# Kernel tuning notes

Hardware: AMD Instinct MI355X
Metric: run time of the kernel (lower is better)

Reference implementation:

```python
import jax, jax.numpy as jnp
import numpy as np

EMBED = 128      # embed_dim
D2 = 128         # state_dim_2d
ENC = 128        # encoder_state_dim
L_IN = 64        # max_input_len
L_OUT = 64       # max_output_len
VOCAB = 32000
BATCH = 32
CELL_IN = 2 * ENC + EMBED  # 384


def setup_inputs() -> dict:
    key = jax.random.key(0)
    ks = jax.random.split(key, 17)
    w = lambda k, shape: jax.random.normal(k, shape, jnp.float32) * 0.05
    return {
        "x": jax.random.randint(ks[0], (L_IN, BATCH), 0, VOCAB),
        "embedding": w(ks[1], (VOCAB, EMBED)),
        # bidirectional encoder LSTM, torch gate order (i, f, g, o)
        "enc_Wih_f": w(ks[2], (4 * ENC, EMBED)),
        "enc_Whh_f": w(ks[3], (4 * ENC, ENC)),
        "enc_bih_f": w(ks[4], (4 * ENC,)),
        "enc_bhh_f": w(ks[5], (4 * ENC,)),
        "enc_Wih_b": w(ks[6], (4 * ENC, EMBED)),
        "enc_Whh_b": w(ks[7], (4 * ENC, ENC)),
        "enc_bih_b": w(ks[8], (4 * ENC,)),
        "enc_bhh_b": w(ks[9], (4 * ENC,)),
        # 2D-LSTM cell: gates (i, f, o, lambda, g)
        "Wx": w(ks[10], (5 * D2, CELL_IN)),
        "bx": w(ks[11], (5 * D2,)),
        "Ws": w(ks[12], (5 * D2, 2 * D2)),
        "bs": w(ks[13], (5 * D2,)),
        "logW": w(ks[14], (VOCAB, D2)),
        "logb": w(ks[15], (VOCAB,)),
    }


def _forward(x, embedding, enc_Wih_f, enc_Whh_f, enc_bih_f, enc_bhh_f,
             enc_Wih_b, enc_Whh_b, enc_bih_b, enc_bhh_b,
             Wx, bx, Ws, bs, logW, logb):
    emb = embedding[x]  # [L_in, B, E]
    Lin, B = emb.shape[0], emb.shape[1]

    def lstm_dir(Wih, Whh, bih, bhh, reverse):
        H = Whh.shape[1]
        def step(carry, e):
            h, c = carry
            z = e @ Wih.T + bih + h @ Whh.T + bhh
            i, f, g, o = jnp.split(z, 4, axis=-1)
            c = jax.nn.sigmoid(f) * c + jax.nn.sigmoid(i) * jnp.tanh(g)
            h = jax.nn.sigmoid(o) * jnp.tanh(c)
            return (h, c), h
        init = (jnp.zeros((B, H), emb.dtype), jnp.zeros((B, H), emb.dtype))
        _, hs = jax.lax.scan(step, init, emb, reverse=reverse)
        return hs

    # bidirectional encoder hidden states: [L_in, B, 2*ENC]
    h = jnp.concatenate([
        lstm_dir(enc_Wih_f, enc_Whh_f, enc_bih_f, enc_bhh_f, False),
        lstm_dir(enc_Wih_b, enc_Whh_b, enc_bih_b, enc_bhh_b, True),
    ], axis=-1)

    D = Ws.shape[1] // 2

    def cell(y_i, h_j, s_hor, s_ver, c_hor, c_ver):
        xj = jnp.concatenate([y_i, h_j], axis=-1)
        z = xj @ Wx.T + bx + jnp.concatenate([s_hor, s_ver], axis=-1) @ Ws.T + bs
        i, f, o, l, g = jnp.split(z, 5, axis=-1)
        i, f, o, l = (jax.nn.sigmoid(t) for t in (i, f, o, l))
        g = jnp.tanh(g)
        c = f * (l * c_hor + (1.0 - l) * c_ver) + i * g
        s = o * jnp.tanh(c)
        return c, s

    z0 = jnp.zeros((B, D), h.dtype)
    zrow = jnp.zeros((Lin, B, D), h.dtype)
    y0 = jnp.zeros((B, embedding.shape[1]), h.dtype)

    def outer(carry, _):
        y_i, s_row, c_row = carry
        def inner(hc, inp):
            s_hor, c_hor = hc
            h_j, s_ver, c_ver = inp
            c, s = cell(y_i, h_j, s_hor, s_ver, c_hor, c_ver)
            return (s, c), (s, c)
        (s_last, _), (s_new, c_new) = jax.lax.scan(inner, (z0, z0), (h, s_row, c_row))
        probs = jax.nn.softmax(s_last @ logW.T + logb, axis=-1)
        y_next = embedding[jnp.argmax(probs, axis=-1)]
        return (y_next, s_new, c_new), probs

    _, y_hat = jax.lax.scan(outer, (y0, zrow, zrow), None, length=L_OUT)
    return y_hat  # [L_out, B, V]


def reference(x, embedding, enc_Wih_f, enc_Whh_f, enc_bih_f, enc_bhh_f,
              enc_Wih_b, enc_Whh_b, enc_bih_b, enc_bhh_b,
              Wx, bx, Ws, bs, logW, logb):
    return _forward(x, embedding, enc_Wih_f, enc_Whh_f, enc_bih_f, enc_bhh_f,
                    enc_Wih_b, enc_Whh_b, enc_bih_b, enc_bhh_b,
                    Wx, bx, Ws, bs, logW, logb)
```

## Files before the change

kernel.cpp:

```cpp
#include <hip/hip_runtime.h>
#include <cstdint>
#include <cstddef>

#define LI 64
#define LO 64
#define NB 32
#define E  128
#define ENC 128
#define D2 128
#define VOC 32000
#define CIN 384
#define G5 640
#define G4 512
#define NCK 256
#define VPC 125

__device__ __forceinline__ float sigf(float x) { return 1.0f / (1.0f + __expf(-x)); }
__device__ __forceinline__ float tanhf_(float x) {
  float e = __expf(2.0f * x);
  return 1.0f - 2.0f / (e + 1.0f);
}

__global__ __launch_bounds__(512) void k_embed_encpre(
    const int* __restrict__ x, const float* __restrict__ embed,
    const float* __restrict__ Wf, const float* __restrict__ bihf, const float* __restrict__ bhhf,
    const float* __restrict__ Wb, const float* __restrict__ bihb, const float* __restrict__ bhhb,
    float* __restrict__ Xf, float* __restrict__ Xb)
{
  int t = blockIdx.x >> 2, bg = (blockIdx.x & 3) * 8;
  __shared__ float4 embs[8][E/4];
  int tid = threadIdx.x;
  for (int idx = tid; idx < 8 * E; idx += 512) {
    int bb = idx >> 7, e = idx & 127;
    int tok = x[t * NB + bg + bb];
    ((float*)embs[bb])[e] = embed[(size_t)tok * E + e];
  }
  __syncthreads();
  int gd = tid;
  for (int dir = 0; dir < 2; ++dir) {
    const float4* wrow = (const float4*)((dir ? Wb : Wf) + (size_t)gd * E);
    float bias = dir ? (bihb[gd] + bhhb[gd]) : (bihf[gd] + bhhf[gd]);
    float acc[8];
    #pragma unroll
    for (int r = 0; r < 8; ++r) acc[r] = bias;
    for (int q = 0; q < E/4; ++q) {
      float4 w = wrow[q];
      #pragma unroll
      for (int r = 0; r < 8; ++r) {
        float4 e4 = embs[r][q];
        acc[r] += w.x*e4.x + w.y*e4.y + w.z*e4.z + w.w*e4.w;
      }
    }
    float* X = dir ? Xb : Xf;
    #pragma unroll
    for (int r = 0; r < 8; ++r)
      X[(size_t)(t * NB + bg + r) * G4 + gd] = acc[r];
  }
}

__global__ __launch_bounds__(512) void k_encoder(
    const float* __restrict__ Xf, const float* __restrict__ Xb,
    const float* __restrict__ Whhf, const float* __restrict__ Whhb,
    float* __restrict__ henc)
{
  int b = blockIdx.x >> 1, dir = blockIdx.x & 1;
  const float* X   = dir ? Xb   : Xf;
  const float* Whh = dir ? Whhb : Whhf;
  int tid = threadIdx.x;
  float4 w[ENC/4];
  {
    const float4* wrow = (const float4*)(Whh + (size_t)tid * ENC);
    #pragma unroll
    for (int q = 0; q < ENC/4; ++q) w[q] = wrow[q];
  }
  __shared__ float4 hb4[ENC/4];
  __shared__ float zb[G4];
  if (tid < ENC/4) hb4[tid] = make_float4(0.f, 0.f, 0.f, 0.f);
  float c = 0.0f;
  __syncthreads();
  for (int st = 0; st < LI; ++st) {
    int t = dir ? (LI - 1 - st) : st;
    float acc = X[(size_t)(t * NB + b) * G4 + tid];
    #pragma unroll
    for (int q = 0; q < ENC/4; ++q) {
      float4 h4 = hb4[q];
      float4 ww = w[q];
      acc += ww.x*h4.x + ww.y*h4.y + ww.z*h4.z + ww.w*h4.w;
    }
    zb[tid] = acc;
    __syncthreads();
    if (tid < ENC) {
      float zi = zb[tid], zf = zb[ENC + tid], zg = zb[2*ENC + tid], zo = zb[3*ENC + tid];
      c = sigf(zf) * c + sigf(zi) * tanhf_(zg);
      float h = sigf(zo) * tanhf_(c);
      ((float*)hb4)[tid] = h;
      henc[(size_t)(t * NB + b) * (2*ENC) + dir*ENC + tid] = h;
    }
    __syncthreads();
  }
}

__global__ __launch_bounds__(640) void k_hx(
    const float* __restrict__ henc, const float* __restrict__ Wx,
    const float* __restrict__ bx, const float* __restrict__ bs,
    float* __restrict__ Hx, float* __restrict__ Vpre0)
{
  int rowbase = blockIdx.x * 8;
  __shared__ float4 hh[8][(2*ENC)/4];
  int tid = threadIdx.x;
  for (int idx = tid; idx < 8 * 2 * ENC; idx += 640) {
    int rr = idx >> 8, k = idx & 255;
    ((float*)hh[rr])[k] = henc[(size_t)(rowbase + rr) * (2*ENC) + k];
  }
  __syncthreads();
  int gd = tid;
  const float4* wrow = (const float4*)(Wx + (size_t)gd * CIN + E);
  float bias = bx[gd] + bs[gd];
  float acc[8];
  #pragma unroll
  for (int r = 0; r < 8; ++r) acc[r] = bias;
  for (int q = 0; q < (2*ENC)/4; ++q) {
    float4 w = wrow[q];
    #pragma unroll
    for (int r = 0; r < 8; ++r) {
      float4 h4 = hh[r][q];
      acc[r] += w.x*h4.x + w.y*h4.y + w.z*h4.z + w.w*h4.w;
    }
  }
  #pragma unroll
  for (int r = 0; r < 8; ++r) {
    size_t o = (size_t)(rowbase + r) * G5 + gd;
    Hx[o] = acc[r];
    Vpre0[o] = acc[r];
  }
}

__global__ __launch_bounds__(640) void k_row(
    int row,
    const float* __restrict__ embed, const float* __restrict__ Wx,
    const float* __restrict__ Ws,
    const float* __restrict__ Vpre,
    const float* __restrict__ cprev,
    float* __restrict__ scur, float* __restrict__ ccur,
    const float* __restrict__ ckval, const int* __restrict__ ckidx)
{
  int b = blockIdx.x, tid = threadIdx.x;
  __shared__ float zb[G5];
  __shared__ float4 sb4[D2/4];
  __shared__ float ybuf[E];
  __shared__ int tokls;
  float yxr = 0.0f;
  if (row > 0) {
    if (tid < 64) {
      float bv = -3.4e38f; int bi = 0x7fffffff;
      #pragma unroll
      for (int cc = 0; cc < 4; ++cc) {
        int c = tid + 64 * cc;
        float v = ckval[b * NCK + c];
        int   id = ckidx[b * NCK + c];
        if (v > bv || (v == bv && id < bi)) { bv = v; bi = id; }
      }
      #pragma unroll
      for (int off = 1; off < 64; off <<= 1) {
        float ov = __shfl_xor(bv, off);
        int   oi = __shfl_xor(bi, off);
        if (ov > bv || (ov == bv && oi < bi)) { bv = ov; bi = oi; }
      }
      if (tid == 0) tokls = bi;
    }
    __syncthreads();
    int tok = tokls;
    if (tid < E) ybuf[tid] = embed[(size_t)tok * E + tid];
    __syncthreads();
    const float4* wy = (const float4*)(Wx + (size_t)tid * CIN);
    const float4* y4 = (const float4*)ybuf;
    float a = 0.0f;
    #pragma unroll
    for (int q = 0; q < E/4; ++q) {
      float4 w = wy[q], y = y4[q];
      a += w.x*y.x + w.y*y.y + w.z*y.z + w.w*y.w;
    }
    yxr = a;
  }
  float4 w[D2/4];
  {
    const float4* wrow = (const float4*)(Ws + (size_t)tid * (2*D2));
    #pragma unroll
    for (int q = 0; q < D2/4; ++q) w[q] = wrow[q];
  }
  if (tid < D2/4) sb4[tid] = make_float4(0.f, 0.f, 0.f, 0.f);
  float chor = 0.0f;
  __syncthreads();
  float vnext = Vpre[(size_t)(0 * NB + b) * G5 + tid];
  float cvn = (tid < D2) ? cprev[(size_t)(0 * NB + b) * D2 + tid] : 0.0f;
  for (int j = 0; j < LI; ++j) {
    float acc = yxr + vnext;
    if (j < LI - 1) vnext = Vpre[(size_t)((j + 1) * NB + b) * G5 + tid];
    #pragma unroll
    for (int q = 0; q < D2/4; ++q) {
      float4 s4 = sb4[q];
      float4 ww = w[q];
      acc += ww.x*s4.x + ww.y*s4.y + ww.z*s4.z + ww.w*s4.w;
    }
    zb[tid] = acc;
    __syncthreads();
    if (tid < D2) {
      float zi = zb[tid], zf = zb[D2 + tid], zo = zb[2*D2 + tid],
            zl = zb[3*D2 + tid], zg = zb[4*D2 + tid];
      float cv = cvn;
      if (j < LI - 1) cvn = cprev[(size_t)((j + 1) * NB + b) * D2 + tid];
      float ii = sigf(zi), ff = sigf(zf), oo = sigf(zo), ll = sigf(zl);
      float gg = tanhf_(zg);
      float c = ff * (ll * chor + (1.0f - ll) * cv) + ii * gg;
      float s = oo * tanhf_(c);
      chor = c;
      ((float*)sb4)[tid] = s;
      size_t o = (size_t)(j * NB + b) * D2 + tid;
      ccur[o] = c;
      scur[o] = s;
    }
    __syncthreads();
  }
}

__global__ __launch_bounds__(256) void k_fused(
    int row,
    const float* __restrict__ scur,
    const float* __restrict__ logW, const float* __restrict__ logb,
    const float* __restrict__ Ws, const float* __restrict__ Hx,
    float* __restrict__ Vnxt,
    float* __restrict__ lgcur, float* __restrict__ ckvalcur, int* __restrict__ ckidxcur,
    const float* __restrict__ lgprev, const float* __restrict__ ckvalprev,
    float* __restrict__ dout)
{
  int bid = blockIdx.x, tid = threadIdx.x;
  if (bid < 256) {
    if (row >= 64) return;
    int b = tid >> 3, r = tid & 7;
    const float4* sp = (const float4*)(scur + (size_t)(63 * NB + b) * D2 + r * 16);
    float4 s0 = sp[0], s1 = sp[1], s2 = sp[2], s3 = sp[3];
    float bm = -3.4e38f; int bmi = 0;
    int v0 = bid * VPC;
    for (int k = 0; k < VPC; ++k) {
      int v = v0 + k;
      const float4* lw = (const float4*)(logW + (size_t)v * D2 + r * 16);
      float4 a0 = lw[0], a1 = lw[1], a2 = lw[2], a3 = lw[3];
      float sum = a0.x*s0.x + a0.y*s0.y + a0.z*s0.z + a0.w*s0.w
                + a1.x*s1.x + a1.y*s1.y + a1.z*s1.z + a1.w*s1.w
                + a2.x*s2.x + a2.y*s2.y + a2.z*s2.z + a2.w*s2.w
                + a3.x*s3.x + a3.y*s3.y + a3.z*s3.z + a3.w*s3.w;
      sum += __shfl_xor(sum, 1);
      sum += __shfl_xor(sum, 2);
      sum += __shfl_xor(sum, 4);
      if (r == 0) {
        float lg = sum + logb[v];
        lgcur[(size_t)b * VOC + v] = lg;
        if (lg > bm) { bm = lg; bmi = v; }
      }
    }
    if (r == 0) {
      ckvalcur[b * NCK + bid] = bm;
      ckidxcur[b * NCK + bid] = bmi;
    }
  } else if (bid < 512) {
    if (row >= 63) return;
    int rowbase = (bid - 256) * 8;
    __shared__ float4 sr[8][D2/4];
    for (int idx = tid; idx < 8 * D2; idx += 256) {
      int rr = idx >> 7, k = idx & 127;
      ((float*)sr[rr])[k] = scur[(size_t)(rowbase + rr) * D2 + k];
    }
    __syncthreads();
    for (int gd = tid; gd < G5; gd += 256) {
      const float4* wrow = (const float4*)(Ws + (size_t)gd * (2*D2) + D2);
      float acc[8];
      #pragma unroll
      for (int rr = 0; rr < 8; ++rr) acc[rr] = 0.0f;
      for (int q = 0; q < D2/4; ++q) {
        float4 ww = wrow[q];
        #pragma unroll
        for (int rr = 0; rr < 8; ++rr) {
          float4 s4 = sr[rr][q];
          acc[rr] += ww.x*s4.x + ww.y*s4.y + ww.z*s4.z + ww.w*s4.w;
        }
      }
      #pragma unroll
      for (int rr = 0; rr < 8; ++rr) {
        size_t o = (size_t)(rowbase + rr) * G5 + gd;
        Vnxt[o] = Hx[o] + acc[rr];
      }
    }
  } else {
    if (row == 0) return;
    int b = bid - 512;
    __shared__ float red[256];
    red[tid] = ckvalprev[b * NCK + tid];
    __syncthreads();
    for (int off = 128; off > 0; off >>= 1) {
      if (tid < off) red[tid] = fmaxf(red[tid], red[tid + off]);
      __syncthreads();
    }
    float M = red[0];
    __syncthreads();
    const float* lg = lgprev + (size_t)b * VOC;
    float S = 0.0f;
    for (int k = 0; k < VPC; ++k) S += __expf(lg[tid + 256 * k] - M);
    red[tid] = S;
    __syncthreads();
    for (int off = 128; off > 0; off >>= 1) {
      if (tid < off) red[tid] += red[tid + off];
      __syncthreads();
    }
    float rinv = 1.0f / red[0];
    float* o = dout + ((size_t)(row - 1) * NB + b) * VOC;
    for (int k = 0; k < VPC; ++k) {
      int v = tid + 256 * k;
      o[v] = __expf(lg[v] - M) * rinv;
    }
  }
}

extern "C" void kernel_launch(void* const* d_in, const int* in_sizes, int n_in,
                              void* d_out, int out_size, void* d_ws, size_t ws_size,
                              hipStream_t stream)
{
  (void)in_sizes; (void)n_in; (void)out_size; (void)ws_size;
  const int*   x     = (const int*)d_in[0];
  const float* embed = (const float*)d_in[1];
  const float* Wihf  = (const float*)d_in[2];
  const float* Whhf  = (const float*)d_in[3];
  const float* bihf  = (const float*)d_in[4];
  const float* bhhf  = (const float*)d_in[5];
  const float* Wihb  = (const float*)d_in[6];
  const float* Whhb  = (const float*)d_in[7];
  const float* bihb  = (const float*)d_in[8];
  const float* bhhb  = (const float*)d_in[9];
  const float* Wx    = (const float*)d_in[10];
  const float* bx    = (const float*)d_in[11];
  const float* Ws    = (const float*)d_in[12];
  const float* bs    = (const float*)d_in[13];
  const float* logW  = (const float*)d_in[14];
  const float* logb  = (const float*)d_in[15];
  float* out = (float*)d_out;

  float* w    = (float*)d_ws;
  float* Xf   = w;
  float* Xb   = Xf   + 1048576;
  float* henc = Xb   + 1048576;
  float* Hx   = henc + 524288;
  float* Vpre = Hx   + 1310720;
  float* SC   = Vpre + 2621440;
  float* lg   = SC   + 1048576;
  float* ckv  = lg   + 2048000;
  int*   cki  = (int*)(ckv + 16384);

  hipMemsetAsync(SC + 524288, 0, (size_t)524288 * sizeof(float), stream);

  k_embed_encpre<<<256, 512, 0, stream>>>(x, embed, Wihf, bihf, bhhf,
                                          Wihb, bihb, bhhb, Xf, Xb);
  k_encoder<<<64, 512, 0, stream>>>(Xf, Xb, Whhf, Whhb, henc);
  k_hx<<<256, 640, 0, stream>>>(henc, Wx, bx, bs, Hx, Vpre );

  for (int i = 0; i <= 64; ++i) {
    int cur = i & 1, prv = (i + 1) & 1;
    float* scur  = SC + (size_t)cur * 524288;
    float* ccur  = scur + 262144;
    float* sprev = SC + (size_t)prv * 524288;
    float* cprev = sprev + 262144;
    if (i < 64) {
      k_row<<<32, 640, 0, stream>>>(i, embed, Wx, Ws,
          Vpre + (size_t)cur * 1310720, cprev, scur, ccur,
          ckv + (size_t)prv * 8192, cki + (size_t)prv * 8192);
    }
    k_fused<<<544, 256, 0, stream>>>(i, scur, logW, logb, Ws, Hx,
        Vpre + (size_t)prv * 1310720,
        lg + (size_t)cur * 1024000, ckv + (size_t)cur * 8192, cki + (size_t)cur * 8192,
        lg + (size_t)prv * 1024000, ckv + (size_t)prv * 8192,
        out);
  }
}
```

Before: 11.25 ms.

## Merge all stages into one persistent kernel synchronized by global atomic flags

Replaces the sequence of about 130 kernel launches (embedding, encoder, Hx projection, then per-row row/fused kernels) with a single persistent kernel of 256 blocks. Stages are ordered through per-stage atomic counters in workspace, with spin-waiting on acquire loads. The softmax for the previous row is moved onto idle blocks so it overlaps with the next row's recurrence. The encoder and row dot products are also split into four independent accumulators. This removes launch gaps and inter-kernel drain, but relies on all 256 blocks being co-resident. Idle blocks now spin on global flags.

New measurement: 27.17 ms. 142% more time.

```diff
diff --git a/kernel.cpp b/kernel.cpp
--- a/kernel.cpp
+++ b/kernel.cpp
@@ -3,7 +3,6 @@
 #include <cstddef>
 
 #define LI 64
-#define LO 64
 #define NB 32
 #define E  128
 #define ENC 128
@@ -14,6 +13,25 @@
 #define G4 512
 #define NCK 256
 #define VPC 125
+#define TPB 640
+#define NBLK 256
+
+#define OFF_XF    0
+#define OFF_XB    1048576
+#define OFF_HENC  2097152
+#define OFF_HX    2621440
+#define OFF_VPRE  3932160
+#define OFF_SC    6553600
+#define OFF_LG    7602176
+#define OFF_CKV   9650176
+#define OFF_CKI   9666560
+#define OFF_FLAGS 9682944
+
+#define F_EMBED 0
+#define F_ENC   1
+#define F_HX    2
+#define F_ROW   3
+#define F_POST  67
 
 __device__ __forceinline__ float sigf(float x) { return 1.0f / (1.0f + __expf(-x)); }
 __device__ __forceinline__ float tanhf_(float x) {
@@ -21,302 +39,349 @@
   return 1.0f - 2.0f / (e + 1.0f);
 }
 
-__global__ __launch_bounds__(512) void k_embed_encpre(
+__device__ __forceinline__ void fwait(int* f, int tgt) {
+  if (threadIdx.x == 0) {
+    while (__hip_atomic_load(f, __ATOMIC_ACQUIRE, __HIP_MEMORY_SCOPE_AGENT) < tgt)
+      __builtin_amdgcn_s_sleep(2);
+  }
+  __syncthreads();
+}
+__device__ __forceinline__ void fadd(int* f) {
+  __syncthreads();
+  if (threadIdx.x == 0)
+    (void)__hip_atomic_fetch_add(f, 1, __ATOMIC_RELEASE, __HIP_MEMORY_SCOPE_AGENT);
+}
+
+__device__ void softmax_write(int r, int b, const float* __restrict__ LG,
+                              const float* __restrict__ CKV,
+                              float* __restrict__ out, float* s_red)
+{
+  int tid = threadIdx.x;
+  const float* lgr  = LG + (size_t)(r & 1) * 1024000 + (size_t)b * VOC;
+  const float* ckvr = CKV + (size_t)(r & 1) * 8192 + b * NCK;
+  if (tid < 256) s_red[tid] = ckvr[tid];
+  __syncthreads();
+  for (int off = 128; off > 0; off >>= 1) {
+    if (tid < off) s_red[tid] = fmaxf(s_red[tid], s_red[tid + off]);
+    __syncthreads();
+  }
+  float M = s_red[0];
+  __syncthreads();
+  float S = 0.0f;
+  if (tid < 256) {
+    for (int k = 0; k < VPC; ++k) S += __expf(lgr[tid + 256 * k] - M);
+    s_red[tid] = S;
+  }
+  __syncthreads();
+  for (int off = 128; off > 0; off >>= 1) {
+    if (tid < off) s_red[tid] += s_red[tid + off];
+    __syncthreads();
+  }
+  float rinv = 1.0f / s_red[0];
+  float* o = out + ((size_t)r * NB + b) * VOC;
+  for (int v = tid; v < VOC; v += TPB)
+    o[v] = __expf(lgr[v] - M) * rinv;
+  __syncthreads();
+}
+
+__global__ __launch_bounds__(TPB) void mega(
     const int* __restrict__ x, const float* __restrict__ embed,
-    const float* __restrict__ Wf, const float* __restrict__ bihf, const float* __restrict__ bhhf,
-    const float* __restrict__ Wb, const float* __restrict__ bihb, const float* __restrict__ bhhb,
-    float* __restrict__ Xf, float* __restrict__ Xb)
+    const float* __restrict__ Wihf, const float* __restrict__ Whhf,
+    const float* __restrict__ bihf, const float* __restrict__ bhhf,
+    const float* __restrict__ Wihb, const float* __restrict__ Whhb,
+    const float* __restrict__ bihb, const float* __restrict__ bhhb,
+    const float* __restrict__ Wx, const float* __restrict__ bx,
+    const float* __restrict__ Ws, const float* __restrict__ bs,
+    const float* __restrict__ logW, const float* __restrict__ logb,
+    float* __restrict__ ws, int* __restrict__ F, float* __restrict__ out)
 {
-  int t = blockIdx.x >> 2, bg = (blockIdx.x & 3) * 8;
-  __shared__ float4 embs[8][E/4];
-  int tid = threadIdx.x;
-  for (int idx = tid; idx < 8 * E; idx += 512) {
-    int bb = idx >> 7, e = idx & 127;
-    int tok = x[t * NB + bg + bb];
-    ((float*)embs[bb])[e] = embed[(size_t)tok * E + e];
-  }
-  __syncthreads();
-  int gd = tid;
-  for (int dir = 0; dir < 2; ++dir) {
-    const float4* wrow = (const float4*)((dir ? Wb : Wf) + (size_t)gd * E);
-    float bias = dir ? (bihb[gd] + bhhb[gd]) : (bihf[gd] + bhhf[gd]);
+  __shared__ float LB[24576];
+  float* s_embs = LB;
+  float* s_hh   = LB;
+  float* s_zbE  = LB;
+  float* s_hb   = LB + 512;
+  float* s_zb   = LB;
+  float* s_sb   = LB + 640;
+  float* s_yb   = LB + 768;
+  int*   s_tok  = (int*)(LB + 896);
+  float* s_red  = LB;
+  float* s_sr   = LB;
+
+  float* Xf   = ws + OFF_XF;
+  float* Xb   = ws + OFF_XB;
+  float* henc = ws + OFF_HENC;
+  float* Hx   = ws + OFF_HX;
+  float* Vpre = ws + OFF_VPRE;
+  float* SC   = ws + OFF_SC;
+  float* LG   = ws + OFF_LG;
+  float* CKV  = ws + OFF_CKV;
+  int*   CKI  = (int*)(ws + OFF_CKI);
+
+  int bid = blockIdx.x, tid = threadIdx.x;
+
+  {
+    int t = bid >> 2, bg = (bid & 3) * 8;
+    for (int idx = tid; idx < 8 * E; idx += TPB) {
+      int bb = idx >> 7, e = idx & 127;
+      int tok = x[t * NB + bg + bb];
+      s_embs[bb * E + e] = embed[(size_t)tok * E + e];
+    }
+    __syncthreads();
+    if (tid < G4) {
+      for (int dir = 0; dir < 2; ++dir) {
+        const float4* wrow = (const float4*)((dir ? Wihb : Wihf) + (size_t)tid * E);
+        float bias = dir ? (bihb[tid] + bhhb[tid]) : (bihf[tid] + bhhf[tid]);
+        float acc[8];
+        #pragma unroll
+        for (int r = 0; r < 8; ++r) acc[r] = bias;
+        for (int q = 0; q < E / 4; ++q) {
+          float4 w = wrow[q];
+          #pragma unroll
+          for (int r = 0; r < 8; ++r) {
+            float4 e4 = ((const float4*)(s_embs + r * E))[q];
+            acc[r] += w.x * e4.x + w.y * e4.y + w.z * e4.z + w.w * e4.w;
+          }
+        }
+        float* X = dir ? Xb : Xf;
+        #pragma unroll
+        for (int r = 0; r < 8; ++r)
+          X[(size_t)(t * NB + bg + r) * G4 + tid] = acc[r];
+      }
+    }
+    fadd(&F[F_EMBED]);
+  }
+
+  if (bid < 64) {
+    fwait(&F[F_EMBED], NBLK);
+    int b = bid >> 1, dir = bid & 1;
+    const float* X   = dir ? Xb : Xf;
+    const float* Whh = dir ? Whhb : Whhf;
+    float4 w[ENC / 4];
+    if (tid < G4) {
+      const float4* wrow = (const float4*)(Whh + (size_t)tid * ENC);
+      #pragma unroll
+      for (int q = 0; q < ENC / 4; ++q) w[q] = wrow[q];
+    }
+    if (tid < ENC / 4) ((float4*)s_hb)[tid] = make_float4(0.f, 0.f, 0.f, 0.f);
+    float c = 0.0f;
+    __syncthreads();
+    for (int st = 0; st < LI; ++st) {
+      int t = dir ? (LI - 1 - st) : st;
+      if (tid < G4) {
+        float a0 = X[(size_t)(t * NB + b) * G4 + tid], a1 = 0.f, a2 = 0.f, a3 = 0.f;
+        const float4* hb4 = (const float4*)s_hb;
+        #pragma unroll
+        for (int q = 0; q < ENC / 4; q += 4) {
+          float4 h0 = hb4[q], h1 = hb4[q + 1], h2 = hb4[q + 2], h3 = hb4[q + 3];
+          a0 += w[q].x * h0.x + w[q].y * h0.y + w[q].z * h0.z + w[q].w * h0.w;
+          a1 += w[q+1].x * h1.x + w[q+1].y * h1.y + w[q+1].z * h1.z + w[q+1].w * h1.w;
+          a2 += w[q+2].x * h2.x + w[q+2].y * h2.y + w[q+2].z * h2.z + w[q+2].w * h2.w;
+          a3 += w[q+3].x * h3.x + w[q+3].y * h3.y + w[q+3].z * h3.z + w[q+3].w * h3.w;
+        }
+        s_zbE[tid] = (a0 + a1) + (a2 + a3);
+      }
+      __syncthreads();
+      if (tid < ENC) {
+        float zi = s_zbE[tid], zf = s_zbE[ENC + tid],
+              zg = s_zbE[2 * ENC + tid], zo = s_zbE[3 * ENC + tid];
+        c = sigf(zf) * c + sigf(zi) * tanhf_(zg);
+        float h = sigf(zo) * tanhf_(c);
+        s_hb[tid] = h;
+        henc[(size_t)(t * NB + b) * (2 * ENC) + dir * ENC + tid] = h;
+      }
+      __syncthreads();
+    }
+    fadd(&F[F_ENC]);
+  }
+
+  {
+    fwait(&F[F_ENC], 64);
+    int rowbase = bid * 8;
+    for (int idx = tid; idx < 8 * 2 * ENC; idx += TPB) {
+      int rr = idx >> 8, k = idx & 255;
+      s_hh[rr * 256 + k] = henc[(size_t)(rowbase + rr) * (2 * ENC) + k];
+    }
+    __syncthreads();
+    const float4* wrow = (const float4*)(Wx + (size_t)tid * CIN + E);
+    float bias = bx[tid] + bs[tid];
     float acc[8];
     #pragma unroll
     for (int r = 0; r < 8; ++r) acc[r] = bias;
-    for (int q = 0; q < E/4; ++q) {
+    for (int q = 0; q < (2 * ENC) / 4; ++q) {
       float4 w = wrow[q];
       #pragma unroll
       for (int r = 0; r < 8; ++r) {
-        float4 e4 = embs[r][q];
-        acc[r] += w.x*e4.x + w.y*e4.y + w.z*e4.z + w.w*e4.w;
-      }
-    }
-    float* X = dir ? Xb : Xf;
-    #pragma unroll
-    for (int r = 0; r < 8; ++r)
-      X[(size_t)(t * NB + bg + r) * G4 + gd] = acc[r];
-  }
-}
-
-__global__ __launch_bounds__(512) void k_encoder(
-    const float* __restrict__ Xf, const float* __restrict__ Xb,
-    const float* __restrict__ Whhf, const float* __restrict__ Whhb,
-    float* __restrict__ henc)
-{
-  int b = blockIdx.x >> 1, dir = blockIdx.x & 1;
-  const float* X   = dir ? Xb   : Xf;
-  const float* Whh = dir ? Whhb : Whhf;
-  int tid = threadIdx.x;
-  float4 w[ENC/4];
-  {
-    const float4* wrow = (const float4*)(Whh + (size_t)tid * ENC);
-    #pragma unroll
-    for (int q = 0; q < ENC/4; ++q) w[q] = wrow[q];
-  }
-  __shared__ float4 hb4[ENC/4];
-  __shared__ float zb[G4];
-  if (tid < ENC/4) hb4[tid] = make_float4(0.f, 0.f, 0.f, 0.f);
-  float c = 0.0f;
-  __syncthreads();
-  for (int st = 0; st < LI; ++st) {
-    int t = dir ? (LI - 1 - st) : st;
-    float acc = X[(size_t)(t * NB + b) * G4 + tid];
-    #pragma unroll
-    for (int q = 0; q < ENC/4; ++q) {
-      float4 h4 = hb4[q];
-      float4 ww = w[q];
-      acc += ww.x*h4.x + ww.y*h4.y + ww.z*h4.z + ww.w*h4.w;
-    }
-    zb[tid] = acc;
-    __syncthreads();
-    if (tid < ENC) {
-      float zi = zb[tid], zf = zb[ENC + tid], zg = zb[2*ENC + tid], zo = zb[3*ENC + tid];
-      c = sigf(zf) * c + sigf(zi) * tanhf_(zg);
-      float h = sigf(zo) * tanhf_(c);
-      ((float*)hb4)[tid] = h;
-      henc[(size_t)(t * NB + b) * (2*ENC) + dir*ENC + tid] = h;
-    }
-    __syncthreads();
-  }
-}
-
-__global__ __launch_bounds__(640) void k_hx(
-    const float* __restrict__ henc, const float* __restrict__ Wx,
-    const float* __restrict__ bx, const float* __restrict__ bs,
-    float* __restrict__ Hx, float* __restrict__ Vpre0)
-{
-  int rowbase = blockIdx.x * 8;
-  __shared__ float4 hh[8][(2*ENC)/4];
-  int tid = threadIdx.x;
-  for (int idx = tid; idx < 8 * 2 * ENC; idx += 640) {
-    int rr = idx >> 8, k = idx & 255;
-    ((float*)hh[rr])[k] = henc[(size_t)(rowbase + rr) * (2*ENC) + k];
-  }
-  __syncthreads();
-  int gd = tid;
-  const float4* wrow = (const float4*)(Wx + (size_t)gd * CIN + E);
-  float bias = bx[gd] + bs[gd];
-  float acc[8];
-  #pragma unroll
-  for (int r = 0; r < 8; ++r) acc[r] = bias;
-  for (int q = 0; q < (2*ENC)/4; ++q) {
-    float4 w = wrow[q];
+        float4 h4 = ((const float4*)(s_hh + r * 256))[q];
+        acc[r] += w.x * h4.x + w.y * h4.y + w.z * h4.z + w.w * h4.w;
+      }
+    }
     #pragma unroll
     for (int r = 0; r < 8; ++r) {
-      float4 h4 = hh[r][q];
-      acc[r] += w.x*h4.x + w.y*h4.y + w.z*h4.z + w.w*h4.w;
-    }
-  }
-  #pragma unroll
-  for (int r = 0; r < 8; ++r) {
-    size_t o = (size_t)(rowbase + r) * G5 + gd;
-    Hx[o] = acc[r];
-    Vpre0[o] = acc[r];
-  }
-}
-
-__global__ __launch_bounds__(640) void k_row(
-    int row,
-    const float* __restrict__ embed, const float* __restrict__ Wx,
-    const float* __restrict__ Ws,
-    const float* __restrict__ Vpre,
-    const float* __restrict__ cprev,
-    float* __restrict__ scur, float* __restrict__ ccur,
-    const float* __restrict__ ckval, const int* __restrict__ ckidx)
-{
-  int b = blockIdx.x, tid = threadIdx.x;
-  __shared__ float zb[G5];
-  __shared__ float4 sb4[D2/4];
-  __shared__ float ybuf[E];
-  __shared__ int tokls;
-  float yxr = 0.0f;
-  if (row > 0) {
-    if (tid < 64) {
-      float bv = -3.4e38f; int bi = 0x7fffffff;
-      #pragma unroll
-      for (int cc = 0; cc < 4; ++cc) {
-        int c = tid + 64 * cc;
-        float v = ckval[b * NCK + c];
-        int   id = ckidx[b * NCK + c];
-        if (v > bv || (v == bv && id < bi)) { bv = v; bi = id; }
-      }
-      #pragma unroll
-      for (int off = 1; off < 64; off <<= 1) {
-        float ov = __shfl_xor(bv, off);
-        int   oi = __shfl_xor(bi, off);
-        if (ov > bv || (ov == bv && oi < bi)) { bv = ov; bi = oi; }
-      }
-      if (tid == 0) tokls = bi;
-    }
-    __syncthreads();
-    int tok = tokls;
-    if (tid < E) ybuf[tid] = embed[(size_t)tok * E + tid];
-    __syncthreads();
-    const float4* wy = (const float4*)(Wx + (size_t)tid * CIN);
-    const float4* y4 = (const float4*)ybuf;
-    float a = 0.0f;
-    #pragma unroll
-    for (int q = 0; q < E/4; ++q) {
-      float4 w = wy[q], y = y4[q];
-      a += w.x*y.x + w.y*y.y + w.z*y.z + w.w*y.w;
-    }
-    yxr = a;
-  }
-  float4 w[D2/4];
-  {
-    const float4* wrow = (const float4*)(Ws + (size_t)tid * (2*D2));
-    #pragma unroll
-    for (int q = 0; q < D2/4; ++q) w[q] = wrow[q];
-  }
-  if (tid < D2/4) sb4[tid] = make_float4(0.f, 0.f, 0.f, 0.f);
-  float chor = 0.0f;
-  __syncthreads();
-  float vnext = Vpre[(size_t)(0 * NB + b) * G5 + tid];
-  float cvn = (tid < D2) ? cprev[(size_t)(0 * NB + b) * D2 + tid] : 0.0f;
-  for (int j = 0; j < LI; ++j) {
-    float acc = yxr + vnext;
-    if (j < LI - 1) vnext = Vpre[(size_t)((j + 1) * NB + b) * G5 + tid];
-    #pragma unroll
-    for (int q = 0; q < D2/4; ++q) {
-      float4 s4 = sb4[q];
-      float4 ww = w[q];
-      acc += ww.x*s4.x + ww.y*s4.y + ww.z*s4.z + ww.w*s4.w;
-    }
-    zb[tid] = acc;
-    __syncthreads();
-    if (tid < D2) {
-      float zi = zb[tid], zf = zb[D2 + tid], zo = zb[2*D2 + tid],
-            zl = zb[3*D2 + tid], zg = zb[4*D2 + tid];
-      float cv = cvn;
-      if (j < LI - 1) cvn = cprev[(size_t)((j + 1) * NB + b) * D2 + tid];
-      float ii = sigf(zi), ff = sigf(zf), oo = sigf(zo), ll = sigf(zl);
-      float gg = tanhf_(zg);
-      float c = ff * (ll * chor + (1.0f - ll) * cv) + ii * gg;
-      float s = oo * tanhf_(c);
-      chor = c;
-      ((float*)sb4)[tid] = s;
-      size_t o = (size_t)(j * NB + b) * D2 + tid;
-      ccur[o] = c;
-      scur[o] = s;
-    }
-    __syncthreads();
-  }
-}
-
-__global__ __launch_bounds__(256) void k_fused(
-    int row,
-    const float* __restrict__ scur,
-    const float* __restrict__ logW, const float* __restrict__ logb,
-    const float* __restrict__ Ws, const float* __restrict__ Hx,
-    float* __restrict__ Vnxt,
-    float* __restrict__ lgcur, float* __restrict__ ckvalcur, int* __restrict__ ckidxcur,
-    const float* __restrict__ lgprev, const float* __restrict__ ckvalprev,
-    float* __restrict__ dout)
-{
-  int bid = blockIdx.x, tid = threadIdx.x;
-  if (bid < 256) {
-    if (row >= 64) return;
-    int b = tid >> 3, r = tid & 7;
-    const float4* sp = (const float4*)(scur + (size_t)(63 * NB + b) * D2 + r * 16);
-    float4 s0 = sp[0], s1 = sp[1], s2 = sp[2], s3 = sp[3];
-    float bm = -3.4e38f; int bmi = 0;
-    int v0 = bid * VPC;
-    for (int k = 0; k < VPC; ++k) {
-      int v = v0 + k;
-      const float4* lw = (const float4*)(logW + (size_t)v * D2 + r * 16);
-      float4 a0 = lw[0], a1 = lw[1], a2 = lw[2], a3 = lw[3];
-      float sum = a0.x*s0.x + a0.y*s0.y + a0.z*s0.z + a0.w*s0.w
-                + a1.x*s1.x + a1.y*s1.y + a1.z*s1.z + a1.w*s1.w
-                + a2.x*s2.x + a2.y*s2.y + a2.z*s2.z + a2.w*s2.w
-                + a3.x*s3.x + a3.y*s3.y + a3.z*s3.z + a3.w*s3.w;
-      sum += __shfl_xor(sum, 1);
-      sum += __shfl_xor(sum, 2);
-      sum += __shfl_xor(sum, 4);
+      size_t o = (size_t)(rowbase + r) * G5 + tid;
+      Hx[o] = acc[r];
+      Vpre[o] = acc[r];
+    }
+    fadd(&F[F_HX]);
+  }
+
+  for (int i = 0; i < 64; ++i) {
+    float* scur  = SC + (size_t)(i & 1) * 524288;
+    float* ccur  = scur + 262144;
+    float* cprev = SC + (size_t)((i + 1) & 1) * 524288 + 262144;
+    const float* Vp = Vpre + (size_t)(i & 1) * 1310720;
+
+    if (bid < 32) {
+      if (i == 0) fwait(&F[F_HX], NBLK); else fwait(&F[F_POST + i - 1], NBLK);
+      int b = bid;
+      float yxr = 0.0f;
+      if (i > 0) {
+        const float* ckv = CKV + (size_t)((i + 1) & 1) * 8192;
+        const int*   cki = CKI + (size_t)((i + 1) & 1) * 8192;
+        if (tid < 64) {
+          float bv = -3.4e38f; int bi = 0x7fffffff;
+          #pragma unroll
+          for (int cc = 0; cc < 4; ++cc) {
+            int c = tid + 64 * cc;
+            float v = ckv[b * NCK + c];
+            int  id = cki[b * NCK + c];
+            if (v > bv || (v == bv && id < bi)) { bv = v; bi = id; }
+          }
+          #pragma unroll
+          for (int off = 1; off < 64; off <<= 1) {
+            float ov = __shfl_xor(bv, off);
+            int   oi = __shfl_xor(bi, off);
+            if (ov > bv || (ov == bv && oi < bi)) { bv = ov; bi = oi; }
+          }
+          if (tid == 0) *s_tok = bi;
+        }
+        __syncthreads();
+        int tok = *s_tok;
+        if (tid < E) s_yb[tid] = embed[(size_t)tok * E + tid];
+        __syncthreads();
+        const float4* wy = (const float4*)(Wx + (size_t)tid * CIN);
+        const float4* y4 = (const float4*)s_yb;
+        float a = 0.0f;
+        #pragma unroll
+        for (int q = 0; q < E / 4; ++q) {
+          float4 w = wy[q], y = y4[q];
+          a += w.x * y.x + w.y * y.y + w.z * y.z + w.w * y.w;
+        }
+        yxr = a;
+      }
+      float4 w[D2 / 4];
+      {
+        const float4* wrow = (const float4*)(Ws + (size_t)tid * (2 * D2));
+        #pragma unroll
+        for (int q = 0; q < D2 / 4; ++q) w[q] = wrow[q];
+      }
+      if (tid < D2 / 4) ((float4*)s_sb)[tid] = make_float4(0.f, 0.f, 0.f, 0.f);
+      float chor = 0.0f;
+      __syncthreads();
+      float vnext = Vp[(size_t)(0 * NB + b) * G5 + tid];
+      float cvn = (tid < D2) ? cprev[(size_t)(0 * NB + b) * D2 + tid] : 0.0f;
+      for (int j = 0; j < LI; ++j) {
+        float a0 = yxr + vnext, a1 = 0.f, a2 = 0.f, a3 = 0.f;
+        if (j < LI - 1) vnext = Vp[(size_t)((j + 1) * NB + b) * G5 + tid];
+        const float4* sb4 = (const float4*)s_sb;
+        #pragma unroll
+        for (int q = 0; q < D2 / 4; q += 4) {
+          float4 s0 = sb4[q], s1 = sb4[q + 1], s2 = sb4[q + 2], s3 = sb4[q + 3];
+          a0 += w[q].x * s0.x + w[q].y * s0.y + w[q].z * s0.z + w[q].w * s0.w;
+          a1 += w[q+1].x * s1.x + w[q+1].y * s1.y + w[q+1].z * s1.z + w[q+1].w * s1.w;
+          a2 += w[q+2].x * s2.x + w[q+2].y * s2.y + w[q+2].z * s2.z + w[q+2].w * s2.w;
+          a3 += w[q+3].x * s3.x + w[q+3].y * s3.y + w[q+3].z * s3.z + w[q+3].w * s3.w;
+        }
+        s_zb[tid] = (a0 + a1) + (a2 + a3);
+        __syncthreads();
+        if (tid < D2) {
+          float zi = s_zb[tid], zf = s_zb[D2 + tid], zo = s_zb[2 * D2 + tid],
+                zl = s_zb[3 * D2 + tid], zg = s_zb[4 * D2 + tid];
+          float cv = cvn;
+          if (j < LI - 1) cvn = cprev[(size_t)((j + 1) * NB + b) * D2 + tid];
+          float ii = sigf(zi), ff = sigf(zf), oo = sigf(zo), ll = sigf(zl);
+          float gg = tanhf_(zg);
+          float c = ff * (ll * chor + (1.0f - ll) * cv) + ii * gg;
+          float s = oo * tanhf_(c);
+          chor = c;
+          s_sb[tid] = s;
+          size_t o = (size_t)(j * NB + b) * D2 + tid;
+          ccur[o] = c;
+          scur[o] = s;
+        }
+        __syncthreads();
+      }
+      fadd(&F[F_ROW + i]);
+    } else if (bid < 64) {
+      if (i >= 1) {
+        fwait(&F[F_POST + i - 1], NBLK);
+        softmax_write(i - 1, bid - 32, LG, CKV, out, s_red);
+      }
+    }
+
+    fwait(&F[F_ROW + i], 32);
+    for (int idx = tid; idx < 8 * D2; idx += TPB) {
+      int rr = idx >> 7, k = idx & 127;
+      s_sr[rr * D2 + k] = scur[(size_t)(bid * 8 + rr) * D2 + k];
+    }
+    __syncthreads();
+    if (tid < 256) {
+      int b = tid >> 3, r = tid & 7;
+      const float4* sp = (const float4*)(scur + (size_t)(63 * NB + b) * D2 + r * 16);
+      float4 s0 = sp[0], s1 = sp[1], s2 = sp[2], s3 = sp[3];
+      float bm = -3.4e38f; int bmi = 0;
+      int v0 = bid * VPC;
+      float* lgcur = LG + (size_t)(i & 1) * 1024000;
+      for (int k = 0; k < VPC; ++k) {
+        int v = v0 + k;
+        const float4* lw = (const float4*)(logW + (size_t)v * D2 + r * 16);
+        float4 a0 = lw[0], a1 = lw[1], a2 = lw[2], a3 = lw[3];
+        float sum = a0.x*s0.x + a0.y*s0.y + a0.z*s0.z + a0.w*s0.w
+                  + a1.x*s1.x + a1.y*s1.y + a1.z*s1.z + a1.w*s1.w
+                  + a2.x*s2.x + a2.y*s2.y + a2.z*s2.z + a2.w*s2.w
+                  + a3.x*s3.x + a3.y*s3.y + a3.z*s3.z + a3.w*s3.w;
+        sum += __shfl_xor(sum, 1);
+        sum += __shfl_xor(sum, 2);
+        sum += __shfl_xor(sum, 4);
+        if (r == 0) {
+          float lgv = sum + logb[v];
+          lgcur[(size_t)b * VOC + v] = lgv;
+          if (lgv > bm) { bm = lgv; bmi = v; }
+        }
+      }
       if (r == 0) {
-        float lg = sum + logb[v];
-        lgcur[(size_t)b * VOC + v] = lg;
-        if (lg > bm) { bm = lg; bmi = v; }
-      }
-    }
-    if (r == 0) {
-      ckvalcur[b * NCK + bid] = bm;
-      ckidxcur[b * NCK + bid] = bmi;
-    }
-  } else if (bid < 512) {
-    if (row >= 63) return;
-    int rowbase = (bid - 256) * 8;
-    __shared__ float4 sr[8][D2/4];
-    for (int idx = tid; idx < 8 * D2; idx += 256) {
-      int rr = idx >> 7, k = idx & 127;
-      ((float*)sr[rr])[k] = scur[(size_t)(rowbase + rr) * D2 + k];
-    }
-    __syncthreads();
-    for (int gd = tid; gd < G5; gd += 256) {
-      const float4* wrow = (const float4*)(Ws + (size_t)gd * (2*D2) + D2);
-      float acc[8];
-      #pragma unroll
-      for (int rr = 0; rr < 8; ++rr) acc[rr] = 0.0f;
-      for (int q = 0; q < D2/4; ++q) {
-        float4 ww = wrow[q];
+        CKV[(size_t)(i & 1) * 8192 + b * NCK + bid] = bm;
+        CKI[(size_t)(i & 1) * 8192 + b * NCK + bid] = bmi;
+      }
+    } else if (tid < 512 && i < 63) {
+      int t2 = tid - 256;
+      float* Vnxt = Vpre + (size_t)((i + 1) & 1) * 1310720;
+      int rowbase = bid * 8;
+      for (int gd = t2; gd < G5; gd += 256) {
+        const float4* wrow = (const float4*)(Ws + (size_t)gd * (2 * D2) + D2);
+        float acc[8];
+        #pragma unroll
+        for (int rr = 0; rr < 8; ++rr) acc[rr] = 0.0f;
+        for (int q = 0; q < D2 / 4; ++q) {
+          float4 ww = wrow[q];
+          #pragma unroll
+          for (int rr = 0; rr < 8; ++rr) {
+            float4 s4 = ((const float4*)(s_sr + rr * D2))[q];
+            acc[rr] += ww.x * s4.x + ww.y * s4.y + ww.z * s4.z + ww.w * s4.w;
+          }
+        }
         #pragma unroll
         for (int rr = 0; rr < 8; ++rr) {
-          float4 s4 = sr[rr][q];
-          acc[rr] += ww.x*s4.x + ww.y*s4.y + ww.z*s4.z + ww.w*s4.w;
-        }
-      }
-      #pragma unroll
-      for (int rr = 0; rr < 8; ++rr) {
-        size_t o = (size_t)(rowbase + rr) * G5 + gd;
-        Vnxt[o] = Hx[o] + acc[rr];
-      }
-    }
-  } else {
-    if (row == 0) return;
-    int b = bid - 512;
-    __shared__ float red[256];
-    red[tid] = ckvalprev[b * NCK + tid];
-    __syncthreads();
-    for (int off = 128; off > 0; off >>= 1) {
-      if (tid < off) red[tid] = fmaxf(red[tid], red[tid + off]);
-      __syncthreads();
-    }
-    float M = red[0];
-    __syncthreads();
-    const float* lg = lgprev + (size_t)b * VOC;
-    float S = 0.0f;
-    for (int k = 0; k < VPC; ++k) S += __expf(lg[tid + 256 * k] - M);
-    red[tid] = S;
-    __syncthreads();
-    for (int off = 128; off > 0; off >>= 1) {
-      if (tid < off) red[tid] += red[tid + off];
-      __syncthreads();
-    }
-    float rinv = 1.0f / red[0];
-    float* o = dout + ((size_t)(row - 1) * NB + b) * VOC;
-    for (int k = 0; k < VPC; ++k) {
-      int v = tid + 256 * k;
-      o[v] = __expf(lg[v] - M) * rinv;
-    }
+          size_t o = (size_t)(rowbase + rr) * G5 + gd;
+          Vnxt[o] = Hx[o] + acc[rr];
+        }
+      }
+    }
+    fadd(&F[F_POST + i]);
+  }
+
+  if (bid >= 32 && bid < 64) {
+    fwait(&F[F_POST + 63], NBLK);
+    softmax_write(63, bid - 32, LG, CKV, out, s_red);
   }
 }
 
@@ -342,40 +407,14 @@
   const float* logW  = (const float*)d_in[14];
   const float* logb  = (const float*)d_in[15];
   float* out = (float*)d_out;
-
-  float* w    = (float*)d_ws;
-  float* Xf   = w;
-  float* Xb   = Xf   + 1048576;
-  float* henc = Xb   + 1048576;
-  float* Hx   = henc + 524288;
-  float* Vpre = Hx   + 1310720;
-  float* SC   = Vpre + 2621440;
-  float* lg   = SC   + 1048576;
-  float* ckv  = lg   + 2048000;
-  int*   cki  = (int*)(ckv + 16384);
-
-  hipMemsetAsync(SC + 524288, 0, (size_t)524288 * sizeof(float), stream);
-
-  k_embed_encpre<<<256, 512, 0, stream>>>(x, embed, Wihf, bihf, bhhf,
-                                          Wihb, bihb, bhhb, Xf, Xb);
-  k_encoder<<<64, 512, 0, stream>>>(Xf, Xb, Whhf, Whhb, henc);
-  k_hx<<<256, 640, 0, stream>>>(henc, Wx, bx, bs, Hx, Vpre );
-
-  for (int i = 0; i <= 64; ++i) {
-    int cur = i & 1, prv = (i + 1) & 1;
-    float* scur  = SC + (size_t)cur * 524288;
-    float* ccur  = scur + 262144;
-    float* sprev = SC + (size_t)prv * 524288;
-    float* cprev = sprev + 262144;
-    if (i < 64) {
-      k_row<<<32, 640, 0, stream>>>(i, embed, Wx, Ws,
-          Vpre + (size_t)cur * 1310720, cprev, scur, ccur,
-          ckv + (size_t)prv * 8192, cki + (size_t)prv * 8192);
-    }
-    k_fused<<<544, 256, 0, stream>>>(i, scur, logW, logb, Ws, Hx,
-        Vpre + (size_t)prv * 1310720,
-        lg + (size_t)cur * 1024000, ckv + (size_t)cur * 8192, cki + (size_t)cur * 8192,
-        lg + (size_t)prv * 1024000, ckv + (size_t)prv * 8192,
-        out);
-  }
-}
+  float* w   = (float*)d_ws;
+  int* flags = (int*)(w + OFF_FLAGS);
+
+  hipMemsetAsync(flags, 0, 256 * sizeof(int), stream);
+  hipMemsetAsync(w + OFF_SC + 3 * 262144, 0, 262144 * sizeof(float), stream);
+
+  mega<<<NBLK, TPB, 0, stream>>>(x, embed, Wihf, Whhf, bihf, bhhf,
+                                 Wihb, Whhb, bihb, bhhb,
+                                 Wx, bx, Ws, bs, logW, logb,
+                                 w, flags, out);
+}
```
